# Kernel tuning notes

Hardware: AMD Instinct MI355X
Metric: run time of the kernel (lower is better)

Reference implementation:

```python
import jax, jax.numpy as jnp
import numpy as np

EMBED = 2048
HEADS = 16
GROUPS = 4
HEAD_DIM = EMBED // HEADS  # 128
REPEATS = HEADS // GROUPS  # 4


def setup_inputs() -> dict:
    key = jax.random.key(0)
    ks = jax.random.split(key, 9)
    s = 1.0 / np.sqrt(EMBED)
    kv_dim = GROUPS * HEAD_DIM
    return {
        "x": jax.random.normal(ks[0], (2, 2048, EMBED), dtype=jnp.float32),
        "Wq": jax.random.normal(ks[1], (EMBED, EMBED), dtype=jnp.float32) * s,
        "bq": jnp.zeros((EMBED,), dtype=jnp.float32),
        "Wk": jax.random.normal(ks[2], (EMBED, kv_dim), dtype=jnp.float32) * s,
        "bk": jnp.zeros((kv_dim,), dtype=jnp.float32),
        "Wv": jax.random.normal(ks[3], (EMBED, kv_dim), dtype=jnp.float32) * s,
        "bv": jnp.zeros((kv_dim,), dtype=jnp.float32),
        "Wo": jax.random.normal(ks[4], (EMBED, EMBED), dtype=jnp.float32) * s,
        "bo": jnp.zeros((EMBED,), dtype=jnp.float32),
    }


def reference(x, Wq, bq, Wk, bk, Wv, bv, Wo, bo):
    b, t, e = x.shape
    q = x @ Wq + bq                                   # [b,t,e]
    k = x @ Wk + bk                                   # [b,t,g*d]
    v = x @ Wv + bv
    # [b, g, r, t, d] for q; [b, g, t, d] for k,v (repeat_interleave == group-major)
    q = q.reshape(b, t, GROUPS, REPEATS, HEAD_DIM).transpose(0, 2, 3, 1, 4)
    k = k.reshape(b, t, GROUPS, HEAD_DIM).transpose(0, 2, 1, 3)
    v = v.reshape(b, t, GROUPS, HEAD_DIM).transpose(0, 2, 1, 3)
    scale = 1.0 / np.sqrt(HEAD_DIM)
    scores = jnp.einsum('bgrqd,bgkd->bgrqk', q, k) * scale
    causal = jnp.tril(jnp.ones((t, t), dtype=bool))
    scores = jnp.where(causal, scores, -jnp.inf)
    w = jax.nn.softmax(scores, axis=-1)
    out = jnp.einsum('bgrqk,bgkd->bgrqd', w, v)       # [b,g,r,t,d]
    out = out.transpose(0, 3, 1, 2, 4).reshape(b, t, e)
    return out @ Wo + bo
```

## Files before the change

kernel.cpp:

```cpp
#include <hip/hip_runtime.h>
#include <cstdint>

typedef __bf16 bf16;
typedef __attribute__((ext_vector_type(8))) __bf16 bf16x8;
typedef __attribute__((ext_vector_type(4))) __bf16 bf16x4;
typedef __attribute__((ext_vector_type(4))) float f32x4;

__device__ __forceinline__ void load_lds16(const void* g, void* l) {
  __builtin_amdgcn_global_load_lds(
      (const __attribute__((address_space(1))) unsigned int*)g,
      (__attribute__((address_space(3))) unsigned int*)l, 16, 0, 0);
}

__device__ __forceinline__ float fast_exp2(float x) {
  float r;
  asm volatile("v_exp_f32 %0, %1" : "=v"(r) : "v"(x));
  return r;
}

template <bool OUT_F32>
__global__ __launch_bounds__(256) void gemm_bt(
    const bf16* __restrict__ A, const bf16* __restrict__ Bt,
    const float* __restrict__ bias, void* __restrict__ Cv,
    int M, int N, int K) {
  __shared__ __align__(16) bf16 sA[128 * 64];
  __shared__ __align__(16) bf16 sB[128 * 64];
  const int t = threadIdx.x;
  const int w = t >> 6, lane = t & 63;
  const int quad = lane >> 4, l16 = lane & 15;
  const int wm = (w >> 1) * 64, wn = (w & 1) * 64;
  const int bm = blockIdx.y * 128, bn = blockIdx.x * 128;

  f32x4 acc[4][4] = {};
  const int srow = lane >> 3;
  const int sg = lane & 7;

  for (int kt = 0; kt < (K >> 6); ++kt) {
    const int k0 = kt << 6;
#pragma unroll
    for (int c2 = 0; c2 < 4; ++c2) {
      int c = c2 * 4 + w;
      int row = c * 8 + srow;
      int gg = sg ^ (row & 7);
      load_lds16(A + (int64_t)(bm + row) * K + k0 + gg * 8, sA + c * 512);
      load_lds16(Bt + (int64_t)(bn + row) * K + k0 + gg * 8, sB + c * 512);
    }
    asm volatile("s_waitcnt vmcnt(0)" ::: "memory");
    __syncthreads();
#pragma unroll
    for (int ks = 0; ks < 2; ++ks) {
      bf16x8 af[4], bfr[4];
#pragma unroll
      for (int i = 0; i < 4; ++i) {
        int m = wm + i * 16 + l16;
        af[i] = *(const bf16x8*)(sA + m * 64 + (((ks * 4 + quad) ^ (l16 & 7)) * 8));
        int n = wn + i * 16 + l16;
        bfr[i] = *(const bf16x8*)(sB + n * 64 + (((ks * 4 + quad) ^ (l16 & 7)) * 8));
      }
#pragma unroll
      for (int i = 0; i < 4; ++i)
#pragma unroll
        for (int j = 0; j < 4; ++j)
          acc[i][j] = __builtin_amdgcn_mfma_f32_16x16x32_bf16(af[i], bfr[j],
                                                              acc[i][j], 0, 0, 0);
    }
    __syncthreads();
  }
#pragma unroll
  for (int i = 0; i < 4; ++i) {
    int gm = bm + wm + i * 16 + quad * 4;
#pragma unroll
    for (int j = 0; j < 4; ++j) {
      int gn = bn + wn + j * 16 + l16;
      float bvv = bias ? bias[gn] : 0.0f;
#pragma unroll
      for (int r = 0; r < 4; ++r) {
        float v = acc[i][j][r] + bvv;
        if (OUT_F32)
          ((float*)Cv)[(int64_t)(gm + r) * N + gn] = v;
        else
          ((bf16*)Cv)[(int64_t)(gm + r) * N + gn] = (bf16)v;
      }
    }
  }
}

__global__ __launch_bounds__(256, 2) void attn(
    const bf16* __restrict__ QKV, const bf16* __restrict__ Vt,
    bf16* __restrict__ Out) {
  constexpr float CC = 0.08838834764831845f * 1.44269504088896f;
  __shared__ __align__(16) bf16 sK[2][64 * 128];
  __shared__ __align__(16) bf16 sV[2][128 * 64];
  __shared__ __align__(16) bf16 sP[128 * 64];

  const int t = threadIdx.x;
  const int w = t >> 6, lane = t & 63;
  const int quad = lane >> 4, l16 = lane & 15;
  const int p = blockIdx.x, h = blockIdx.y, b = blockIdx.z;
  const int g = h >> 2;
  const int wr0 = w * 16;
  const int kbase = 2048 + g * 128;
  const bf16* vtb = Vt + (int64_t)((b * 4 + g) * 128) * 2048;
  const int rk = lane >> 4, rv = lane >> 3, sgv = lane & 7;
  const int qrow0A = p * 64, qrow0B = (31 - p) * 64;
  const int niters = 32 - p;

  bf16x8 qreg[2][4];
#pragma unroll
  for (int u = 0; u < 2; ++u) {
    int qr = (u == 0 ? qrow0A : qrow0B);
#pragma unroll
    for (int ks = 0; ks < 4; ++ks)
      qreg[u][ks] = *(const bf16x8*)(QKV +
          (int64_t)(b * 2048 + qr + wr0 + l16) * 3072 + h * 128 + ks * 32 +
          quad * 8);
  }

  f32x4 oacc[2][8] = {};
  float mrow[2] = {-3.0e38f, -3.0e38f};
  float lrow[2] = {0.f, 0.f};

  auto stage = [&](int n0, bf16* sKb, bf16* sVb) {
#pragma unroll
    for (int c2 = 0; c2 < 4; ++c2) {
      int c = c2 * 4 + w;
      int rowk = c * 4 + rk;
      int ggk = (l16 & 8) | ((l16 ^ rowk) & 7);
      load_lds16(QKV + (int64_t)(b * 2048 + n0 + rowk) * 3072 + kbase + ggk * 8,
                 sKb + c * 512);
      int rowv = c * 8 + rv;
      int ggv = sgv ^ (rowv & 7);
      load_lds16(vtb + (int64_t)rowv * 2048 + n0 + ggv * 8, sVb + c * 512);
    }
  };

  stage(0, sK[0], sV[0]);

  const int prowA = wr0 + l16;
  const int prowB = 64 + wr0 + l16;

  for (int it = 0; it < niters; ++it) {
    const int cur = it & 1;
    const int n0 = it * 64;
    bf16* sKc = sK[cur];
    bf16* sVc = sV[cur];
    const bool actA = (it <= p);

    asm volatile("s_waitcnt vmcnt(0)\n\ts_barrier" ::: "memory");
    if (it + 1 < niters) stage(n0 + 64, sK[cur ^ 1], sV[cur ^ 1]);

    f32x4 sacc[2][4] = {};
    if (actA) {
#pragma unroll
      for (int ks = 0; ks < 4; ++ks) {
        bf16x8 ak[4];
#pragma unroll
        for (int mj = 0; mj < 4; ++mj) {
          int kvr = mj * 16 + l16;
          int G = ks * 4 + quad;
          int slot = (G & 8) | ((G ^ kvr) & 7);
          ak[mj] = *(const bf16x8*)(sKc + kvr * 128 + slot * 8);
        }
#pragma unroll
        for (int mj = 0; mj < 4; ++mj) {
          sacc[0][mj] = __builtin_amdgcn_mfma_f32_16x16x32_bf16(
              ak[mj], qreg[0][ks], sacc[0][mj], 0, 0, 0);
          sacc[1][mj] = __builtin_amdgcn_mfma_f32_16x16x32_bf16(
              ak[mj], qreg[1][ks], sacc[1][mj], 0, 0, 0);
        }
      }
    } else {
#pragma unroll
      for (int ks = 0; ks < 4; ++ks) {
        bf16x8 ak[4];
#pragma unroll
        for (int mj = 0; mj < 4; ++mj) {
          int kvr = mj * 16 + l16;
          int G = ks * 4 + quad;
          int slot = (G & 8) | ((G ^ kvr) & 7);
          ak[mj] = *(const bf16x8*)(sKc + kvr * 128 + slot * 8);
        }
#pragma unroll
        for (int mj = 0; mj < 4; ++mj)
          sacc[1][mj] = __builtin_amdgcn_mfma_f32_16x16x32_bf16(
              ak[mj], qreg[1][ks], sacc[1][mj], 0, 0, 0);
      }
    }

    auto softmax_u = [&](int u, bool last, int qrow0u, int prow) {
      if (last) {
        int q = qrow0u + wr0 + l16;
#pragma unroll
        for (int mj = 0; mj < 4; ++mj)
#pragma unroll
          for (int r = 0; r < 4; ++r) {
            int kv = n0 + mj * 16 + quad * 4 + r;
            if (kv > q) sacc[u][mj][r] = -3.0e38f;
          }
      }
      f32x4 m01, m23;
#pragma unroll
      for (int r = 0; r < 4; ++r) {
        m01[r] = fmaxf(sacc[u][0][r], sacc[u][1][r]);
        m23[r] = fmaxf(sacc[u][2][r], sacc[u][3][r]);
      }
      float mx = fmaxf(fmaxf(fmaxf(m01[0], m01[1]), fmaxf(m01[2], m01[3])),
                       fmaxf(fmaxf(m23[0], m23[1]), fmaxf(m23[2], m23[3])));
      mx = fmaxf(mx, __shfl_xor(mx, 16));
      mx = fmaxf(mx, __shfl_xor(mx, 32));
      float mnew = fmaxf(mrow[u], mx);
      float alpha = fast_exp2((mrow[u] - mnew) * CC);
      float rs = 0.f;
#pragma unroll
      for (int mj = 0; mj < 4; ++mj) {
        bf16x4 p4;
#pragma unroll
        for (int r = 0; r < 4; ++r) {
          float pv = fast_exp2((sacc[u][mj][r] - mnew) * CC);
          rs += pv;
          p4[r] = (bf16)pv;
        }
        int g16 = mj * 2 + (quad >> 1);
        int off = prow * 64 + ((g16 ^ (prow & 7)) * 8) + (quad & 1) * 4;
        *(bf16x4*)(sP + off) = p4;
      }
      rs += __shfl_xor(rs, 16);
      rs += __shfl_xor(rs, 32);
      lrow[u] = lrow[u] * alpha + rs;
      mrow[u] = mnew;
#pragma unroll
      for (int dj = 0; dj < 8; ++dj)
#pragma unroll
        for (int r = 0; r < 4; ++r) oacc[u][dj][r] *= alpha;
    };
    if (actA) softmax_u(0, it == p, qrow0A, prowA);
    softmax_u(1, it == niters - 1, qrow0B, prowB);

    asm volatile("s_waitcnt lgkmcnt(0)" ::: "memory");

#pragma unroll
    for (int ks2 = 0; ks2 < 2; ++ks2) {
      int G = ks2 * 4 + quad;
      bf16x8 bpA, bpB;
      if (actA)
        bpA = *(const bf16x8*)(sP + prowA * 64 + ((G ^ (prowA & 7)) * 8));
      bpB = *(const bf16x8*)(sP + prowB * 64 + ((G ^ (prowB & 7)) * 8));
      bf16x8 av[8];
#pragma unroll
      for (int dj = 0; dj < 8; ++dj) {
        int d = dj * 16 + l16;
        av[dj] = *(const bf16x8*)(sVc + d * 64 + ((G ^ (d & 7)) * 8));
      }
      if (actA) {
#pragma unroll
        for (int dj = 0; dj < 8; ++dj) {
          oacc[0][dj] = __builtin_amdgcn_mfma_f32_16x16x32_bf16(
              av[dj], bpA, oacc[0][dj], 0, 0, 0);
          oacc[1][dj] = __builtin_amdgcn_mfma_f32_16x16x32_bf16(
              av[dj], bpB, oacc[1][dj], 0, 0, 0);
        }
      } else {
#pragma unroll
        for (int dj = 0; dj < 8; ++dj)
          oacc[1][dj] = __builtin_amdgcn_mfma_f32_16x16x32_bf16(
              av[dj], bpB, oacc[1][dj], 0, 0, 0);
      }
    }
  }

#pragma unroll
  for (int u = 0; u < 2; ++u) {
    int qrow0u = (u == 0 ? qrow0A : qrow0B);
    float inv = 1.0f / lrow[u];
    int64_t grow = b * 2048 + qrow0u + wr0 + l16;
#pragma unroll
    for (int dj = 0; dj < 8; ++dj) {
      bf16x4 o4;
#pragma unroll
      for (int r = 0; r < 4; ++r) o4[r] = (bf16)(oacc[u][dj][r] * inv);
      *(bf16x4*)(Out + grow * 2048 + h * 128 + dj * 16 + quad * 4) = o4;
    }
  }
}

__device__ __forceinline__ void tr_tile(const float* __restrict__ W,
                                        bf16* __restrict__ Wt, int K, int N,
                                        int bx, int by, int t, float* tile) {
  int tx = t & 63, ty = t >> 6;
#pragma unroll
  for (int q2 = 0; q2 < 16; ++q2) {
    int r = ty + q2 * 4;
    tile[r * 65 + tx] = W[(int64_t)(by * 64 + r) * N + bx * 64 + tx];
  }
  __syncthreads();
#pragma unroll
  for (int q2 = 0; q2 < 16; ++q2) {
    int n = ty + q2 * 4;
    Wt[(int64_t)(bx * 64 + n) * K + by * 64 + tx] = (bf16)tile[tx * 65 + n];
  }
}

__global__ __launch_bounds__(256) void prep(
    const float* __restrict__ x, const float* __restrict__ Wq,
    const float* __restrict__ Wk, const float* __restrict__ Wv,
    const float* __restrict__ Wo, const float* __restrict__ bq,
    const float* __restrict__ bk, const float* __restrict__ bv,
    bf16* __restrict__ xb, bf16* __restrict__ wqkvT, bf16* __restrict__ woT,
    float* __restrict__ bqkv) {
  __shared__ float tile[64 * 65];
  const int bid = blockIdx.x;
  const int t = threadIdx.x;
  if (bid < 8192) {
    int idx = bid * 256 + t;
    float4 v = ((const float4*)x)[idx];
    bf16x4 o = {(bf16)v.x, (bf16)v.y, (bf16)v.z, (bf16)v.w};
    ((bf16x4*)xb)[idx] = o;
  } else if (bid < 8192 + 1024) {
    int b2 = bid - 8192;
    tr_tile(Wq, wqkvT, 2048, 2048, b2 & 31, b2 >> 5, t, tile);
  } else if (bid < 8192 + 1024 + 256) {
    int b2 = bid - (8192 + 1024);
    tr_tile(Wk, wqkvT + 2048 * 2048, 2048, 512, b2 & 7, b2 >> 3, t, tile);
  } else if (bid < 8192 + 1024 + 512) {
    int b2 = bid - (8192 + 1024 + 256);
    tr_tile(Wv, wqkvT + 2560 * 2048, 2048, 512, b2 & 7, b2 >> 3, t, tile);
  } else if (bid < 8192 + 1024 + 512 + 1024) {
    int b2 = bid - (8192 + 1024 + 512);
    tr_tile(Wo, woT, 2048, 2048, b2 & 31, b2 >> 5, t, tile);
  } else {
    int i = (bid - (8192 + 1024 + 512 + 1024)) * 256 + t;
    if (i < 3072)
      bqkv[i] = i < 2048 ? bq[i] : (i < 2560 ? bk[i - 2048] : bv[i - 2560]);
  }
}

__global__ void transpose_v(const bf16* __restrict__ QKV, bf16* __restrict__ Vt) {
  __shared__ bf16 tile[32][34];
  int dt = blockIdx.x, tt = blockIdx.y, bg = blockIdx.z;
  int b = bg >> 2, g = bg & 3;
  int tx = threadIdx.x, ty = threadIdx.y;
#pragma unroll
  for (int q2 = 0; q2 < 4; ++q2) {
    int trow = tt * 32 + ty + q2 * 8;
    tile[ty + q2 * 8][tx] =
        QKV[(int64_t)(b * 2048 + trow) * 3072 + 2560 + g * 128 + dt * 32 + tx];
  }
  __syncthreads();
#pragma unroll
  for (int q2 = 0; q2 < 4; ++q2) {
    int d = dt * 32 + ty + q2 * 8;
    Vt[(int64_t)(bg * 128 + d) * 2048 + tt * 32 + tx] = tile[tx][ty + q2 * 8];
  }
}

extern "C" void kernel_launch(void* const* d_in, const int* in_sizes, int n_in,
                              void* d_out, int out_size, void* d_ws,
                              size_t ws_size, hipStream_t stream) {
  const float* x = (const float*)d_in[0];
  const float* Wq = (const float*)d_in[1];
  const float* bq = (const float*)d_in[2];
  const float* Wk = (const float*)d_in[3];
  const float* bk = (const float*)d_in[4];
  const float* Wv = (const float*)d_in[5];
  const float* bv = (const float*)d_in[6];
  const float* Wo = (const float*)d_in[7];
  const float* bo = (const float*)d_in[8];
  float* out = (float*)d_out;

  char* ws = (char*)d_ws;
  bf16* xb = (bf16*)(ws);
  bf16* wqkvT = (bf16*)(ws + 16777216);
  bf16* woT = (bf16*)(ws + 29360128);
  float* bqkv = (float*)(ws + 37748736);
  bf16* qkv = (bf16*)(ws + 37761024);
  bf16* vt = (bf16*)(ws + 62926848);
  bf16* attnb = (bf16*)(ws + 67121152);

  prep<<<8192 + 1024 + 512 + 1024 + 12, 256, 0, stream>>>(
      x, Wq, Wk, Wv, Wo, bq, bk, bv, xb, wqkvT, woT, bqkv);

  gemm_bt<false><<<dim3(24, 32), 256, 0, stream>>>(xb, wqkvT, bqkv, qkv, 4096,
                                                   3072, 2048);
  transpose_v<<<dim3(4, 64, 8), dim3(32, 8), 0, stream>>>(qkv, vt);
  attn<<<dim3(16, 16, 2), 256, 0, stream>>>(qkv, vt, attnb);
  gemm_bt<true><<<dim3(16, 32), 256, 0, stream>>>(attnb, woT, bo, out, 4096,
                                                  2048, 2048);
}
```

Baseline: 306.4 us.

## Restructure attention to single 64-row Q tile per block with 32-wide KV steps

Replaces the paired front/back query-tile scheme with one 64-row query tile per block, doubling the grid and shrinking KV tiles to 32 rows so shared memory and registers drop enough for four blocks per CU. A per-(head-half, batch) remapping of block index to query tile spreads the causal workload. The softmax scale is folded into Q, and the running-max rescale is skipped when the new max exceeds the old by no more than a threshold. The trade-off is more loop iterations with less MFMA work each, plus causal load balancing that now depends on the block scheduler.

```diff
diff --git a/kernel.cpp b/kernel.cpp
--- a/kernel.cpp
+++ b/kernel.cpp
@@ -85,201 +85,161 @@
   }
 }
 
-__global__ __launch_bounds__(256, 2) void attn(
+__global__ __launch_bounds__(256, 4) void attn(
     const bf16* __restrict__ QKV, const bf16* __restrict__ Vt,
     bf16* __restrict__ Out) {
   constexpr float CC = 0.08838834764831845f * 1.44269504088896f;
-  __shared__ __align__(16) bf16 sK[2][64 * 128];
-  __shared__ __align__(16) bf16 sV[2][128 * 64];
-  __shared__ __align__(16) bf16 sP[128 * 64];
+  __shared__ __align__(16) bf16 sK[2][32 * 128];
+  __shared__ __align__(16) bf16 sV[2][128 * 32];
+  __shared__ __align__(16) bf16 sP[64 * 32];
 
   const int t = threadIdx.x;
   const int w = t >> 6, lane = t & 63;
   const int quad = lane >> 4, l16 = lane & 15;
-  const int p = blockIdx.x, h = blockIdx.y, b = blockIdx.z;
+  const int x = blockIdx.x, h = blockIdx.y, b = blockIdx.z;
+  const int sel = ((h >> 3) << 1) | b;
+  int q;
+  switch (sel) {
+    case 0: q = x; break;
+    case 1: q = 31 - x; break;
+    case 2: q = (x + 8) & 31; break;
+    default: q = (55 - x) & 31; break;
+  }
   const int g = h >> 2;
   const int wr0 = w * 16;
   const int kbase = 2048 + g * 128;
   const bf16* vtb = Vt + (int64_t)((b * 4 + g) * 128) * 2048;
-  const int rk = lane >> 4, rv = lane >> 3, sgv = lane & 7;
-  const int qrow0A = p * 64, qrow0B = (31 - p) * 64;
-  const int niters = 32 - p;
-
-  bf16x8 qreg[2][4];
-#pragma unroll
-  for (int u = 0; u < 2; ++u) {
-    int qr = (u == 0 ? qrow0A : qrow0B);
-#pragma unroll
-    for (int ks = 0; ks < 4; ++ks)
-      qreg[u][ks] = *(const bf16x8*)(QKV +
-          (int64_t)(b * 2048 + qr + wr0 + l16) * 3072 + h * 128 + ks * 32 +
-          quad * 8);
-  }
-
-  f32x4 oacc[2][8] = {};
-  float mrow[2] = {-3.0e38f, -3.0e38f};
-  float lrow[2] = {0.f, 0.f};
+  const int rk = lane >> 4;
+  const int rv = lane >> 2;
+  const int sgv = lane & 3;
+  const int qrow0 = q * 64;
+  const int trips = 2 * q + 2;
+  const int prow = wr0 + l16;
 
   auto stage = [&](int n0, bf16* sKb, bf16* sVb) {
 #pragma unroll
-    for (int c2 = 0; c2 < 4; ++c2) {
+    for (int c2 = 0; c2 < 2; ++c2) {
       int c = c2 * 4 + w;
       int rowk = c * 4 + rk;
       int ggk = (l16 & 8) | ((l16 ^ rowk) & 7);
       load_lds16(QKV + (int64_t)(b * 2048 + n0 + rowk) * 3072 + kbase + ggk * 8,
                  sKb + c * 512);
-      int rowv = c * 8 + rv;
-      int ggv = sgv ^ (rowv & 7);
+      int rowv = c * 16 + rv;
+      int ggv = sgv ^ (rowv & 3);
       load_lds16(vtb + (int64_t)rowv * 2048 + n0 + ggv * 8, sVb + c * 512);
     }
   };
 
   stage(0, sK[0], sV[0]);
 
-  const int prowA = wr0 + l16;
-  const int prowB = 64 + wr0 + l16;
-
-  for (int it = 0; it < niters; ++it) {
+  bf16x8 qreg[4];
+#pragma unroll
+  for (int ks = 0; ks < 4; ++ks) {
+    bf16x8 v = *(const bf16x8*)(QKV +
+        (int64_t)(b * 2048 + qrow0 + wr0 + l16) * 3072 + h * 128 + ks * 32 +
+        quad * 8);
+#pragma unroll
+    for (int e = 0; e < 8; ++e) v[e] = (bf16)((float)v[e] * CC);
+    qreg[ks] = v;
+  }
+
+  f32x4 oacc[8] = {};
+  float mrow = -3.0e38f;
+  float lrow = 0.f;
+
+  for (int it = 0; it < trips; ++it) {
     const int cur = it & 1;
-    const int n0 = it * 64;
+    const int n0 = it * 32;
     bf16* sKc = sK[cur];
     bf16* sVc = sV[cur];
-    const bool actA = (it <= p);
 
     asm volatile("s_waitcnt vmcnt(0)\n\ts_barrier" ::: "memory");
-    if (it + 1 < niters) stage(n0 + 64, sK[cur ^ 1], sV[cur ^ 1]);
-
-    f32x4 sacc[2][4] = {};
-    if (actA) {
-#pragma unroll
-      for (int ks = 0; ks < 4; ++ks) {
-        bf16x8 ak[4];
-#pragma unroll
-        for (int mj = 0; mj < 4; ++mj) {
-          int kvr = mj * 16 + l16;
-          int G = ks * 4 + quad;
-          int slot = (G & 8) | ((G ^ kvr) & 7);
-          ak[mj] = *(const bf16x8*)(sKc + kvr * 128 + slot * 8);
+    if (it + 1 < trips) stage(n0 + 32, sK[cur ^ 1], sV[cur ^ 1]);
+
+    f32x4 sacc[2] = {};
+#pragma unroll
+    for (int ks = 0; ks < 4; ++ks) {
+      bf16x8 ak[2];
+#pragma unroll
+      for (int mj = 0; mj < 2; ++mj) {
+        int kvr = mj * 16 + l16;
+        int G = ks * 4 + quad;
+        int slot = (G & 8) | ((G ^ kvr) & 7);
+        ak[mj] = *(const bf16x8*)(sKc + kvr * 128 + slot * 8);
+      }
+#pragma unroll
+      for (int mj = 0; mj < 2; ++mj)
+        sacc[mj] = __builtin_amdgcn_mfma_f32_16x16x32_bf16(ak[mj], qreg[ks],
+                                                           sacc[mj], 0, 0, 0);
+    }
+
+    if (it >= 2 * q) {
+      int qg = qrow0 + wr0 + l16;
+#pragma unroll
+      for (int mj = 0; mj < 2; ++mj)
+#pragma unroll
+        for (int r = 0; r < 4; ++r) {
+          int kv = n0 + mj * 16 + quad * 4 + r;
+          if (kv > qg) sacc[mj][r] = -3.0e38f;
         }
-#pragma unroll
-        for (int mj = 0; mj < 4; ++mj) {
-          sacc[0][mj] = __builtin_amdgcn_mfma_f32_16x16x32_bf16(
-              ak[mj], qreg[0][ks], sacc[0][mj], 0, 0, 0);
-          sacc[1][mj] = __builtin_amdgcn_mfma_f32_16x16x32_bf16(
-              ak[mj], qreg[1][ks], sacc[1][mj], 0, 0, 0);
-        }
+    }
+
+    f32x4 m4;
+#pragma unroll
+    for (int r = 0; r < 4; ++r) m4[r] = fmaxf(sacc[0][r], sacc[1][r]);
+    float mx = fmaxf(fmaxf(m4[0], m4[1]), fmaxf(m4[2], m4[3]));
+    mx = fmaxf(mx, __shfl_xor(mx, 16));
+    mx = fmaxf(mx, __shfl_xor(mx, 32));
+    if (!__all(mx <= mrow + 11.0f)) {
+      float mnew = fmaxf(mrow, mx);
+      float alpha = fast_exp2(mrow - mnew);
+      lrow *= alpha;
+#pragma unroll
+      for (int dj = 0; dj < 8; ++dj)
+#pragma unroll
+        for (int r = 0; r < 4; ++r) oacc[dj][r] *= alpha;
+      mrow = mnew;
+    }
+    float rs = 0.f;
+#pragma unroll
+    for (int mj = 0; mj < 2; ++mj) {
+      bf16x4 p4;
+#pragma unroll
+      for (int r = 0; r < 4; ++r) {
+        float pv = fast_exp2(sacc[mj][r] - mrow);
+        rs += pv;
+        p4[r] = (bf16)pv;
       }
-    } else {
-#pragma unroll
-      for (int ks = 0; ks < 4; ++ks) {
-        bf16x8 ak[4];
-#pragma unroll
-        for (int mj = 0; mj < 4; ++mj) {
-          int kvr = mj * 16 + l16;
-          int G = ks * 4 + quad;
-          int slot = (G & 8) | ((G ^ kvr) & 7);
-          ak[mj] = *(const bf16x8*)(sKc + kvr * 128 + slot * 8);
-        }
-#pragma unroll
-        for (int mj = 0; mj < 4; ++mj)
-          sacc[1][mj] = __builtin_amdgcn_mfma_f32_16x16x32_bf16(
-              ak[mj], qreg[1][ks], sacc[1][mj], 0, 0, 0);
-      }
-    }
-
-    auto softmax_u = [&](int u, bool last, int qrow0u, int prow) {
-      if (last) {
-        int q = qrow0u + wr0 + l16;
-#pragma unroll
-        for (int mj = 0; mj < 4; ++mj)
-#pragma unroll
-          for (int r = 0; r < 4; ++r) {
-            int kv = n0 + mj * 16 + quad * 4 + r;
-            if (kv > q) sacc[u][mj][r] = -3.0e38f;
-          }
-      }
-      f32x4 m01, m23;
-#pragma unroll
-      for (int r = 0; r < 4; ++r) {
-        m01[r] = fmaxf(sacc[u][0][r], sacc[u][1][r]);
-        m23[r] = fmaxf(sacc[u][2][r], sacc[u][3][r]);
-      }
-      float mx = fmaxf(fmaxf(fmaxf(m01[0], m01[1]), fmaxf(m01[2], m01[3])),
-                       fmaxf(fmaxf(m23[0], m23[1]), fmaxf(m23[2], m23[3])));
-      mx = fmaxf(mx, __shfl_xor(mx, 16));
-      mx = fmaxf(mx, __shfl_xor(mx, 32));
-      float mnew = fmaxf(mrow[u], mx);
-      float alpha = fast_exp2((mrow[u] - mnew) * CC);
-      float rs = 0.f;
-#pragma unroll
-      for (int mj = 0; mj < 4; ++mj) {
-        bf16x4 p4;
-#pragma unroll
-        for (int r = 0; r < 4; ++r) {
-          float pv = fast_exp2((sacc[u][mj][r] - mnew) * CC);
-          rs += pv;
-          p4[r] = (bf16)pv;
-        }
-        int g16 = mj * 2 + (quad >> 1);
-        int off = prow * 64 + ((g16 ^ (prow & 7)) * 8) + (quad & 1) * 4;
-        *(bf16x4*)(sP + off) = p4;
-      }
-      rs += __shfl_xor(rs, 16);
-      rs += __shfl_xor(rs, 32);
-      lrow[u] = lrow[u] * alpha + rs;
-      mrow[u] = mnew;
-#pragma unroll
-      for (int dj = 0; dj < 8; ++dj)
-#pragma unroll
-        for (int r = 0; r < 4; ++r) oacc[u][dj][r] *= alpha;
-    };
-    if (actA) softmax_u(0, it == p, qrow0A, prowA);
-    softmax_u(1, it == niters - 1, qrow0B, prowB);
+      int c = 2 * mj + (quad >> 1);
+      *(bf16x4*)(sP + prow * 32 + ((c ^ (prow & 3)) * 8) + (quad & 1) * 4) = p4;
+    }
+    rs += __shfl_xor(rs, 16);
+    rs += __shfl_xor(rs, 32);
+    lrow += rs;
 
     asm volatile("s_waitcnt lgkmcnt(0)" ::: "memory");
 
-#pragma unroll
-    for (int ks2 = 0; ks2 < 2; ++ks2) {
-      int G = ks2 * 4 + quad;
-      bf16x8 bpA, bpB;
-      if (actA)
-        bpA = *(const bf16x8*)(sP + prowA * 64 + ((G ^ (prowA & 7)) * 8));
-      bpB = *(const bf16x8*)(sP + prowB * 64 + ((G ^ (prowB & 7)) * 8));
-      bf16x8 av[8];
-#pragma unroll
-      for (int dj = 0; dj < 8; ++dj) {
-        int d = dj * 16 + l16;
-        av[dj] = *(const bf16x8*)(sVc + d * 64 + ((G ^ (d & 7)) * 8));
-      }
-      if (actA) {
-#pragma unroll
-        for (int dj = 0; dj < 8; ++dj) {
-          oacc[0][dj] = __builtin_amdgcn_mfma_f32_16x16x32_bf16(
-              av[dj], bpA, oacc[0][dj], 0, 0, 0);
-          oacc[1][dj] = __builtin_amdgcn_mfma_f32_16x16x32_bf16(
-              av[dj], bpB, oacc[1][dj], 0, 0, 0);
-        }
-      } else {
-#pragma unroll
-        for (int dj = 0; dj < 8; ++dj)
-          oacc[1][dj] = __builtin_amdgcn_mfma_f32_16x16x32_bf16(
-              av[dj], bpB, oacc[1][dj], 0, 0, 0);
-      }
-    }
-  }
-
-#pragma unroll
-  for (int u = 0; u < 2; ++u) {
-    int qrow0u = (u == 0 ? qrow0A : qrow0B);
-    float inv = 1.0f / lrow[u];
-    int64_t grow = b * 2048 + qrow0u + wr0 + l16;
+    bf16x8 bp = *(const bf16x8*)(sP + prow * 32 + ((quad ^ (prow & 3)) * 8));
+    bf16x8 av[8];
 #pragma unroll
     for (int dj = 0; dj < 8; ++dj) {
-      bf16x4 o4;
-#pragma unroll
-      for (int r = 0; r < 4; ++r) o4[r] = (bf16)(oacc[u][dj][r] * inv);
-      *(bf16x4*)(Out + grow * 2048 + h * 128 + dj * 16 + quad * 4) = o4;
-    }
+      int d = dj * 16 + l16;
+      av[dj] = *(const bf16x8*)(sVc + d * 32 + ((quad ^ (d & 3)) * 8));
+    }
+#pragma unroll
+    for (int dj = 0; dj < 8; ++dj)
+      oacc[dj] = __builtin_amdgcn_mfma_f32_16x16x32_bf16(av[dj], bp, oacc[dj],
+                                                         0, 0, 0);
+  }
+
+  const float inv = 1.0f / lrow;
+  const int64_t grow = b * 2048 + qrow0 + wr0 + l16;
+#pragma unroll
+  for (int dj = 0; dj < 8; ++dj) {
+    bf16x4 o4;
+#pragma unroll
+    for (int r = 0; r < 4; ++r) o4[r] = (bf16)(oacc[dj][r] * inv);
+    *(bf16x4*)(Out + grow * 2048 + h * 128 + dj * 16 + quad * 4) = o4;
   }
 }
 
@@ -382,7 +342,7 @@
   gemm_bt<false><<<dim3(24, 32), 256, 0, stream>>>(xb, wqkvT, bqkv, qkv, 4096,
                                                    3072, 2048);
   transpose_v<<<dim3(4, 64, 8), dim3(32, 8), 0, stream>>>(qkv, vt);
-  attn<<<dim3(16, 16, 2), 256, 0, stream>>>(qkv, vt, attnb);
+  attn<<<dim3(32, 16, 2), 256, 0, stream>>>(qkv, vt, attnb);
   gemm_bt<true><<<dim3(16, 32), 256, 0, stream>>>(attnb, woT, bo, out, 4096,
                                                   2048, 2048);
 }
```

New measurement: 314.3 us. 2.6% more time.
